# Kernel tuning notes

Hardware: AMD Instinct MI355X
Metric: run time of the kernel (lower is better)

Reference implementation:

```python
import jax, jax.numpy as jnp
import numpy as np

B, N, C, H = 8, 1024, 768, 12
D = C // H
HID = 4 * C
MAX_TEXT_LEN = 512
LN_EPS = 1e-5


def _ln(x, g, b):
    mu = jnp.mean(x, axis=-1, keepdims=True)
    var = jnp.mean(jnp.square(x - mu), axis=-1, keepdims=True)
    return (x - mu) * jax.lax.rsqrt(var + LN_EPS) * g + b


def _mlp(x, w1, b1, w2, b2):
    h = jax.nn.gelu(x @ w1.T + b1, approximate=False)
    return h @ w2.T + b2


def setup_inputs() -> dict:
    key = jax.random.key(0)
    ks = jax.random.split(key, 16)
    s = 0.02
    return {
        "x": jax.random.normal(ks[0], (B, N, C), jnp.float32),
        "mask": jax.random.randint(ks[1], (B, N), 0, 2).astype(bool),
        "rel_bias": jax.random.normal(ks[2], (H, N, N), jnp.float32) * s,
        "w_qkv": jax.random.normal(ks[3], (3 * C, C), jnp.float32) * s,
        "q_bias": jnp.zeros((C,), jnp.float32),
        "v_bias": jnp.zeros((C,), jnp.float32),
        "w_proj": jax.random.normal(ks[4], (C, C), jnp.float32) * s,
        "b_proj": jnp.zeros((C,), jnp.float32),
        "ln1_g": jnp.ones((C,), jnp.float32),
        "ln1_b": jnp.zeros((C,), jnp.float32),
        "ln2t_g": jnp.ones((C,), jnp.float32),
        "ln2t_b": jnp.zeros((C,), jnp.float32),
        "ln2i_g": jnp.ones((C,), jnp.float32),
        "ln2i_b": jnp.zeros((C,), jnp.float32),
        "w1t": jax.random.normal(ks[5], (HID, C), jnp.float32) * s,
        "b1t": jnp.zeros((HID,), jnp.float32),
        "w2t": jax.random.normal(ks[6], (C, HID), jnp.float32) * s,
        "b2t": jnp.zeros((C,), jnp.float32),
        "w1i": jax.random.normal(ks[7], (HID, C), jnp.float32) * s,
        "b1i": jnp.zeros((HID,), jnp.float32),
        "w2i": jax.random.normal(ks[8], (C, HID), jnp.float32) * s,
        "b2i": jnp.zeros((C,), jnp.float32),
        "gamma1": jnp.full((C,), 0.1, jnp.float32),
        "gamma2": jnp.full((C,), 0.1, jnp.float32),
    }


def reference(x, mask, rel_bias, w_qkv, q_bias, v_bias, w_proj, b_proj,
              ln1_g, ln1_b, ln2t_g, ln2t_b, ln2i_g, ln2i_b,
              w1t, b1t, w2t, b2t, w1i, b1i, w2i, b2i, gamma1, gamma2):
    # ---- attention branch ----
    h = _ln(x, ln1_g, ln1_b)
    qkv_bias = jnp.concatenate([q_bias, jnp.zeros_like(v_bias), v_bias])
    qkv = h @ w_qkv.T + qkv_bias                      # [B,N,3C]
    qkv = qkv.reshape(B, N, 3, H, D).transpose(2, 0, 3, 1, 4)  # [3,B,H,N,D]
    q, k, v = qkv[0], qkv[1], qkv[2]
    q = q * (D ** -0.5)
    attn = jnp.einsum('bhnd,bhmd->bhnm',
                      q.astype(jnp.float32), k.astype(jnp.float32))
    attn = attn + rel_bias[None]                      # [B,H,N,N]
    attn = jnp.where(mask[:, None, None, :], attn, -jnp.inf)
    attn = jax.nn.softmax(attn, axis=-1).astype(x.dtype)
    out = jnp.einsum('bhnm,bhmd->bhnd', attn, v)
    out = out.transpose(0, 2, 1, 3).reshape(B, N, C)
    out = out @ w_proj.T + b_proj
    x = x + gamma1 * out
    # ---- dual-branch layer-scaled MLP (mlp_vl is None path) ----
    xt = x[:, :MAX_TEXT_LEN]
    xi = x[:, MAX_TEXT_LEN:]
    xt = xt + gamma2 * _mlp(_ln(xt, ln2t_g, ln2t_b), w1t, b1t, w2t, b2t)
    xi = xi + gamma2 * _mlp(_ln(xi, ln2i_g, ln2i_b), w1i, b1i, w2i, b2i)
    return jnp.concatenate([xt, xi], axis=1)
```

## Files before the change

kernel.cpp:

```cpp
#include <hip/hip_runtime.h>
#include <hip/hip_bf16.h>
#include <math.h>

#define B_    8
#define N_TOK 1024
#define C_    768
#define H_    12
#define D_    64
#define HID_  3072

typedef __attribute__((ext_vector_type(4)))  float f32x4;
typedef __attribute__((ext_vector_type(16))) float f32x16;
typedef __attribute__((ext_vector_type(8)))  short s16x8;
typedef __attribute__((ext_vector_type(4)))  unsigned short u16x4;

static __device__ __forceinline__ unsigned short f2bf(float x){
  union { __hip_bfloat16 h; unsigned short u; } cv;
  cv.h = __float2bfloat16(x);
  return cv.u;
}
static __device__ __forceinline__ float bf2f(unsigned short u){
  return __uint_as_float(((unsigned)u) << 16);
}

#define GLOAD_LDS16(gp, lp) \
  __builtin_amdgcn_global_load_lds((const __attribute__((address_space(1))) unsigned int*)(gp), \
                                   (__attribute__((address_space(3))) unsigned int*)(lp), 16, 0, 0)

__global__ __launch_bounds__(256) void k_cvt(const float* __restrict__ src,
                                             unsigned short* __restrict__ dst, int n4){
  int i = blockIdx.x * 256 + threadIdx.x;
  if (i >= n4) return;
  const float4* s4 = (const float4*)src;
  float4 v = s4[i];
  u16x4 r;
  r.x = f2bf(v.x); r.y = f2bf(v.y); r.z = f2bf(v.z); r.w = f2bf(v.w);
  *(u16x4*)(dst + (size_t)i*4) = r;
}

__global__ __launch_bounds__(256) void k_ln1(const float* __restrict__ x,
                                             const float* __restrict__ g,
                                             const float* __restrict__ bta,
                                             unsigned short* __restrict__ out){
  int row  = blockIdx.x*4 + (threadIdx.x >> 6);
  int lane = threadIdx.x & 63;
  const float* xr = x + (size_t)row*C_;
  float v[12]; float s = 0.f;
  #pragma unroll
  for (int i=0;i<12;i++){ v[i] = xr[lane + i*64]; s += v[i]; }
  #pragma unroll
  for (int m=1;m<64;m<<=1) s += __shfl_xor(s, m);
  float mu = s * (1.f/768.f);
  float vs = 0.f;
  #pragma unroll
  for (int i=0;i<12;i++){ float d = v[i]-mu; vs += d*d; }
  #pragma unroll
  for (int m=1;m<64;m<<=1) vs += __shfl_xor(vs, m);
  float rs = rsqrtf(vs*(1.f/768.f) + 1e-5f);
  unsigned short* orow = out + (size_t)row*C_;
  #pragma unroll
  for (int i=0;i<12;i++){ int c = lane + i*64; orow[c] = f2bf((v[i]-mu)*rs*g[c] + bta[c]); }
}

__global__ __launch_bounds__(256) void k_ln2(const float* __restrict__ xmid,
                                             const float* __restrict__ gt, const float* __restrict__ bt,
                                             const float* __restrict__ gi, const float* __restrict__ bi,
                                             unsigned short* __restrict__ outc){
  int row  = blockIdx.x*4 + (threadIdx.x >> 6);
  int lane = threadIdx.x & 63;
  int bb = row >> 10, n = row & 1023;
  const float* G = (n < 512) ? gt : gi;
  const float* Bb = (n < 512) ? bt : bi;
  int crow = (n < 512) ? (bb*512 + n) : (4096 + bb*512 + (n - 512));
  const float* xr = xmid + (size_t)row*C_;
  float v[12]; float s = 0.f;
  #pragma unroll
  for (int i=0;i<12;i++){ v[i] = xr[lane + i*64]; s += v[i]; }
  #pragma unroll
  for (int m=1;m<64;m<<=1) s += __shfl_xor(s, m);
  float mu = s * (1.f/768.f);
  float vs = 0.f;
  #pragma unroll
  for (int i=0;i<12;i++){ float d = v[i]-mu; vs += d*d; }
  #pragma unroll
  for (int m=1;m<64;m<<=1) vs += __shfl_xor(vs, m);
  float rs = rsqrtf(vs*(1.f/768.f) + 1e-5f);
  unsigned short* orow = outc + (size_t)crow*C_;
  #pragma unroll
  for (int i=0;i<12;i++){ int c = lane + i*64; orow[c] = f2bf((v[i]-mu)*rs*G[c] + Bb[c]); }
}

template<int MODE>
__global__ __launch_bounds__(256) void k_gemm(
    const unsigned short* __restrict__ A,
    const unsigned short* __restrict__ Bw,
    int K,
    const float* __restrict__ bias,
    const float* __restrict__ bias2,
    const float* __restrict__ resid,
    const float* __restrict__ gamma,
    unsigned short* __restrict__ out_bf,
    float* __restrict__ out_f,
    int n_off)
{
  __shared__ __align__(16) char smem[32768];
  char* As = smem;
  char* Bs = smem + 16384;
  const int tid = threadIdx.x;
  const int lane = tid & 63, w = tid >> 6;
  const int wr = w >> 1, wc = w & 1;
  const int g16 = lane >> 4, c16 = lane & 15;
  const int row0 = blockIdx.x * 128, col0 = blockIdx.y * 128;

  f32x4 acc[4][4] = {};

  const char* Abase = (const char*)A;
  const char* Bbase = (const char*)Bw;
  const size_t rowbytes = (size_t)K * 2;

  for (int kt = 0; kt < K; kt += 64){
    __syncthreads();
    #pragma unroll
    for (int it = 0; it < 4; it++){
      int L = it*4096 + tid*16;
      int r = L >> 7, cb = L & 127;
      int scb = cb ^ ((r & 7) << 4);
      GLOAD_LDS16(Abase + (size_t)(row0 + r)*rowbytes + (size_t)kt*2 + scb, As + L);
      GLOAD_LDS16(Bbase + (size_t)(col0 + r)*rowbytes + (size_t)kt*2 + scb, Bs + L);
    }
    __syncthreads();

    s16x8 af[2][4], bfr[2][4];
    #pragma unroll
    for (int kk = 0; kk < 2; kk++){
      #pragma unroll
      for (int i = 0; i < 4; i++){
        int ra = wr*64 + i*16 + c16;
        af[kk][i]  = *(const s16x8*)(As + ra*128 + ((kk*64 + g16*16) ^ ((ra & 7) << 4)));
        int rb = wc*64 + i*16 + c16;
        bfr[kk][i] = *(const s16x8*)(Bs + rb*128 + ((kk*64 + g16*16) ^ ((rb & 7) << 4)));
      }
    }
    #pragma unroll
    for (int kk = 0; kk < 2; kk++)
      #pragma unroll
      for (int mi = 0; mi < 4; mi++)
        #pragma unroll
        for (int ni = 0; ni < 4; ni++)
          acc[mi][ni] = __builtin_amdgcn_mfma_f32_16x16x32_bf16(af[kk][mi], bfr[kk][ni], acc[mi][ni], 0, 0, 0);
  }

  #pragma unroll
  for (int mi = 0; mi < 4; mi++){
    int mbase = row0 + wr*64 + mi*16 + g16*4;
    #pragma unroll
    for (int ni = 0; ni < 4; ni++){
      int j = col0 + wc*64 + ni*16 + c16;
      f32x4 a = acc[mi][ni];
      if (MODE == 0){
        int which = j / 768;
        int cj = j - which*768;
        float bs = (which == 0) ? bias[cj] : (which == 2 ? bias2[cj] : 0.f);
        int head = cj >> 6, d = cj & 63;
        #pragma unroll
        for (int r = 0; r < 4; r++){
          int mm = mbase + r;
          int bb = mm >> 10, n = mm & 1023;
          float val = a[r] + bs;
          if (which == 0) val *= 0.125f;
          out_bf[((((size_t)which*B_ + bb)*H_ + head)*N_TOK + n)*D_ + d] = f2bf(val);
        }
      } else if (MODE == 1){
        float gm = gamma[j], bs = bias[j];
        #pragma unroll
        for (int r = 0; r < 4; r++){
          size_t idx = (size_t)(mbase + r)*C_ + j;
          out_f[idx] = resid[idx] + gm*(a[r] + bs);
        }
      } else if (MODE == 2){
        float bs = bias[j];
        #pragma unroll
        for (int r = 0; r < 4; r++){
          float t = a[r] + bs;
          out_bf[(size_t)(mbase + r)*HID_ + j] = f2bf(0.5f*t*(1.f + erff(t*0.70710678118654752f)));
        }
      } else {
        float gm = gamma[j], bs = bias[j];
        #pragma unroll
        for (int r = 0; r < 4; r++){
          int mm = mbase + r;
          int bb = mm >> 9, n = (mm & 511) + n_off;
          size_t idx = ((size_t)bb*N_TOK + n)*C_ + j;
          out_f[idx] = resid[idx] + gm*(a[r] + bs);
        }
      }
    }
  }
}

__global__ __launch_bounds__(256, 2) void k_attn(
    const unsigned short* __restrict__ qb,
    const unsigned short* __restrict__ kb,
    const unsigned short* __restrict__ vb,
    const unsigned short* __restrict__ bias_bf,
    const int* __restrict__ mask,
    unsigned short* __restrict__ outb)
{
  __shared__ __align__(16) char smem[45056];
  char* Vt0 = smem;
  char* Vt1 = smem + 8192;
  char* Ks  = smem + 16384;
  char* Bs  = smem + 24576;
  float* maskf = (float*)(smem + 40960);
  char* Oep = smem;

  int wg = blockIdx.x;
  int x = wg & 7, rest = wg >> 3;
  int qt = rest & 7, gl = rest >> 3;
  int g = gl*8 + x;
  int h = g % 12, bb = g / 12;

  const int tid = threadIdx.x, lane = tid & 63, w = tid >> 6;
  const int l31 = lane & 31, h5 = lane >> 5;
  const size_t bh = (size_t)bb*H_ + h;
  const char* qp = (const char*)(qb + bh*N_TOK*D_);
  const char* kp = (const char*)(kb + bh*N_TOK*D_);
  const unsigned short* vp = vb + bh*N_TOK*D_;
  const char* bp = (const char*)(bias_bf + (size_t)h*N_TOK*N_TOK);
  const int q0 = qt*128;
  const int qrow = q0 + w*32 + l31;
  const int qr = w*32 + l31;

  #pragma unroll
  for (int it = 0; it < 2; it++){
    int L = it*4096 + tid*16; int r = L >> 7, cb = L & 127;
    GLOAD_LDS16(kp + (size_t)r*128 + (cb ^ ((r & 7) << 4)), Ks + L);
  }
  #pragma unroll
  for (int it = 0; it < 4; it++){
    int L = it*4096 + tid*16; int r = L >> 7, cb = L & 127;
    GLOAD_LDS16(bp + (size_t)(q0 + r)*2048 + (cb ^ ((r & 7) << 4)), Bs + L);
  }
  unsigned short vv[16];
  #pragma unroll
  for (int j = 0; j < 16; j++) vv[j] = vp[(size_t)(w*16 + j)*D_ + lane];
  {
    int4 m4 = *(const int4*)(mask + bb*N_TOK + tid*4);
    float4 f4;
    f4.x = m4.x ? 0.f : -1e30f; f4.y = m4.y ? 0.f : -1e30f;
    f4.z = m4.z ? 0.f : -1e30f; f4.w = m4.w ? 0.f : -1e30f;
    *(float4*)(maskf + tid*4) = f4;
  }
  s16x8 qf[4];
  #pragma unroll
  for (int t = 0; t < 4; t++)
    qf[t] = *(const s16x8*)(qp + (size_t)qrow*128 + t*32 + h5*16);
  #pragma unroll
  for (int i = 0; i < 2; i++){
    s16x8 pk;
    #pragma unroll
    for (int e = 0; e < 8; e++) pk[e] = (short)vv[i*8 + e];
    *(s16x8*)(Vt0 + lane*128 + ((w*32 + i*16) ^ ((lane & 7) << 4))) = pk;
  }
  __syncthreads();

  f32x16 oacc[2] = {};
  float mrow = -1e30f, lrow = 0.f;

  for (int t = 0; t < 16; t++){
    const int kt = t*64;
    char* Vbuf = (t & 1) ? Vt1 : Vt0;
    char* Vnxt = (t & 1) ? Vt0 : Vt1;

    s16x8 kfr[2][4];
    #pragma unroll
    for (int ck = 0; ck < 2; ck++)
      #pragma unroll
      for (int tt = 0; tt < 4; tt++)
        kfr[ck][tt] = *(const s16x8*)(Ks + (ck*32 + l31)*128 + ((tt*32 + h5*16) ^ ((l31 & 7) << 4)));
    u16x4 bv[2][4];
    #pragma unroll
    for (int ck = 0; ck < 2; ck++)
      #pragma unroll
      for (int rq = 0; rq < 4; rq++){
        int off = ck*64 + rq*16 + h5*8;
        bv[ck][rq] = *(const u16x4*)(Bs + qr*128 + (off ^ ((qr & 7) << 4)));
      }
    __syncthreads();

    if (t < 15){
      #pragma unroll
      for (int it = 0; it < 2; it++){
        int L = it*4096 + tid*16; int r = L >> 7, cb = L & 127;
        GLOAD_LDS16(kp + (size_t)(kt + 64 + r)*128 + (cb ^ ((r & 7) << 4)), Ks + L);
      }
      #pragma unroll
      for (int it = 0; it < 4; it++){
        int L = it*4096 + tid*16; int r = L >> 7, cb = L & 127;
        GLOAD_LDS16(bp + (size_t)(q0 + r)*2048 + (size_t)(kt + 64)*2 + (cb ^ ((r & 7) << 4)), Bs + L);
      }
      #pragma unroll
      for (int j = 0; j < 16; j++)
        vv[j] = vp[(size_t)(kt + 64 + w*16 + j)*D_ + lane];
    }

    f32x16 sacc[2] = {};
    __builtin_amdgcn_s_setprio(1);
    #pragma unroll
    for (int tt = 0; tt < 4; tt++){
      sacc[0] = __builtin_amdgcn_mfma_f32_32x32x16_bf16(kfr[0][tt], qf[tt], sacc[0], 0, 0, 0);
      sacc[1] = __builtin_amdgcn_mfma_f32_32x32x16_bf16(kfr[1][tt], qf[tt], sacc[1], 0, 0, 0);
    }
    __builtin_amdgcn_s_setprio(0);

    float sv[2][16];
    #pragma unroll
    for (int ck = 0; ck < 2; ck++){
      #pragma unroll
      for (int r = 0; r < 16; r++){
        int kk = ck*32 + (r & 3) + 8*(r >> 2) + 4*h5;
        sv[ck][r] = sacc[ck][r] + bf2f(bv[ck][r >> 2][r & 3]) + maskf[kt + kk];
      }
    }

    float tmax = -1e30f;
    #pragma unroll
    for (int ck = 0; ck < 2; ck++)
      #pragma unroll
      for (int r = 0; r < 16; r++) tmax = fmaxf(tmax, sv[ck][r]);
    tmax = fmaxf(tmax, __shfl_xor(tmax, 32));
    float mnew = fmaxf(mrow, tmax);
    float sc = __expf(mrow - mnew);
    mrow = mnew;
    float ps = 0.f;
    #pragma unroll
    for (int ck = 0; ck < 2; ck++)
      #pragma unroll
      for (int r = 0; r < 16; r++){
        float p = __expf(sv[ck][r] - mnew);
        sv[ck][r] = p;
        ps += p;
      }
    ps += __shfl_xor(ps, 32);
    lrow = lrow*sc + ps;
    #pragma unroll
    for (int dt = 0; dt < 2; dt++)
      #pragma unroll
      for (int r = 0; r < 16; r++) oacc[dt][r] *= sc;

    #pragma unroll
    for (int ck = 0; ck < 2; ck++){
      #pragma unroll
      for (int kh = 0; kh < 2; kh++){
        unsigned wA, wB, wC, wD;
        asm("v_cvt_pk_bf16_f32 %0, %1, %2" : "=v"(wA) : "v"(sv[ck][kh*8+0]), "v"(sv[ck][kh*8+1]));
        asm("v_cvt_pk_bf16_f32 %0, %1, %2" : "=v"(wB) : "v"(sv[ck][kh*8+2]), "v"(sv[ck][kh*8+3]));
        asm("v_cvt_pk_bf16_f32 %0, %1, %2" : "=v"(wC) : "v"(sv[ck][kh*8+4]), "v"(sv[ck][kh*8+5]));
        asm("v_cvt_pk_bf16_f32 %0, %1, %2" : "=v"(wD) : "v"(sv[ck][kh*8+6]), "v"(sv[ck][kh*8+7]));
        unsigned tA = (unsigned)__shfl_xor((int)wA, 32);
        unsigned tB = (unsigned)__shfl_xor((int)wB, 32);
        unsigned tC = (unsigned)__shfl_xor((int)wC, 32);
        unsigned tD = (unsigned)__shfl_xor((int)wD, 32);
        union { unsigned u[4]; s16x8 v; } pu;
        pu.u[0] = h5 ? tC : wA;
        pu.u[1] = h5 ? tD : wB;
        pu.u[2] = h5 ? wC : tA;
        pu.u[3] = h5 ? wD : tB;
        __builtin_amdgcn_s_setprio(1);
        #pragma unroll
        for (int dt = 0; dt < 2; dt++){
          int d = dt*32 + l31;
          s16x8 vf = *(const s16x8*)(Vbuf + d*128 + ((ck*64 + kh*32 + h5*16) ^ ((d & 7) << 4)));
          oacc[dt] = __builtin_amdgcn_mfma_f32_32x32x16_bf16(vf, pu.v, oacc[dt], 0, 0, 0);
        }
        __builtin_amdgcn_s_setprio(0);
      }
    }

    if (t < 15){
      #pragma unroll
      for (int i = 0; i < 2; i++){
        s16x8 pk;
        #pragma unroll
        for (int e = 0; e < 8; e++) pk[e] = (short)vv[i*8 + e];
        *(s16x8*)(Vnxt + lane*128 + ((w*32 + i*16) ^ ((lane & 7) << 4))) = pk;
      }
    }
    __syncthreads();
  }

  float inv = 1.f / lrow;
  char* Ow = Oep + w*8192;
  #pragma unroll
  for (int dt = 0; dt < 2; dt++)
    #pragma unroll
    for (int r = 0; r < 16; r++){
      int d = dt*32 + (r & 3) + 8*(r >> 2) + 4*h5;
      *(float*)(Ow + l31*256 + ((d*4) ^ ((l31 & 7) << 4))) = oacc[dt][r] * inv;
    }
  int q2 = lane >> 1, dh = lane & 1;
  float of[32];
  #pragma unroll
  for (int i = 0; i < 8; i++){
    f32x4 v4 = *(const f32x4*)(Ow + q2*256 + ((dh*128 + i*16) ^ ((q2 & 7) << 4)));
    of[i*4+0] = v4[0]; of[i*4+1] = v4[1]; of[i*4+2] = v4[2]; of[i*4+3] = v4[3];
  }
  unsigned short* orow = outb + ((size_t)bb*N_TOK + q0 + w*32 + q2)*C_ + h*64 + dh*32;
  #pragma unroll
  for (int i = 0; i < 4; i++){
    s16x8 ob;
    #pragma unroll
    for (int e = 0; e < 8; e++) ob[e] = (short)f2bf(of[i*8+e]);
    *(s16x8*)(orow + i*8) = ob;
  }
}

extern "C" void kernel_launch(void* const* d_in, const int* in_sizes, int n_in,
                              void* d_out, int out_size, void* d_ws, size_t ws_size,
                              hipStream_t stream) {
  const float* x      = (const float*)d_in[0];
  const int*   mask   = (const int*)  d_in[1];
  const float* relb   = (const float*)d_in[2];
  const float* w_qkv  = (const float*)d_in[3];
  const float* q_bias = (const float*)d_in[4];
  const float* v_bias = (const float*)d_in[5];
  const float* w_proj = (const float*)d_in[6];
  const float* b_proj = (const float*)d_in[7];
  const float* ln1_g  = (const float*)d_in[8];
  const float* ln1_b  = (const float*)d_in[9];
  const float* ln2t_g = (const float*)d_in[10];
  const float* ln2t_b = (const float*)d_in[11];
  const float* ln2i_g = (const float*)d_in[12];
  const float* ln2i_b = (const float*)d_in[13];
  const float* w1t    = (const float*)d_in[14];
  const float* b1t    = (const float*)d_in[15];
  const float* w2t    = (const float*)d_in[16];
  const float* b2t    = (const float*)d_in[17];
  const float* w1i    = (const float*)d_in[18];
  const float* b1i    = (const float*)d_in[19];
  const float* w2i    = (const float*)d_in[20];
  const float* b2i    = (const float*)d_in[21];
  const float* gamma1 = (const float*)d_in[22];
  const float* gamma2 = (const float*)d_in[23];
  float* out = (float*)d_out;
  char* ws = (char*)d_ws;

  size_t off = 0;
  auto nxt = [&](size_t b){ size_t r = off; off += (b + 255) & ~(size_t)255; return r; };
  unsigned short* wq_bf  = (unsigned short*)(ws + nxt((size_t)3*C_*C_*2));
  unsigned short* wp_bf  = (unsigned short*)(ws + nxt((size_t)C_*C_*2));
  unsigned short* w1t_bf = (unsigned short*)(ws + nxt((size_t)HID_*C_*2));
  unsigned short* w2t_bf = (unsigned short*)(ws + nxt((size_t)HID_*C_*2));
  unsigned short* w1i_bf = (unsigned short*)(ws + nxt((size_t)HID_*C_*2));
  unsigned short* w2i_bf = (unsigned short*)(ws + nxt((size_t)HID_*C_*2));
  unsigned short* hln    = (unsigned short*)(ws + nxt((size_t)B_*N_TOK*C_*2));
  unsigned short* qkv    = (unsigned short*)(ws + nxt((size_t)3*B_*N_TOK*C_*2));
  unsigned short* attno  = (unsigned short*)(ws + nxt((size_t)B_*N_TOK*C_*2));
  float*          xmid   = (float*)(ws + nxt((size_t)B_*N_TOK*C_*4));
  unsigned short* ln2c   = hln;
  unsigned short* hidden = qkv;
  unsigned short* bias_bf = (unsigned short*)xmid;

  k_cvt<<<dim3((3*C_*C_/4 + 255)/256), 256, 0, stream>>>(w_qkv, wq_bf, 3*C_*C_/4);
  k_cvt<<<dim3((C_*C_/4 + 255)/256),   256, 0, stream>>>(w_proj, wp_bf, C_*C_/4);
  k_cvt<<<dim3((HID_*C_/4 + 255)/256), 256, 0, stream>>>(w1t, w1t_bf, HID_*C_/4);
  k_cvt<<<dim3((HID_*C_/4 + 255)/256), 256, 0, stream>>>(w2t, w2t_bf, HID_*C_/4);
  k_cvt<<<dim3((HID_*C_/4 + 255)/256), 256, 0, stream>>>(w1i, w1i_bf, HID_*C_/4);
  k_cvt<<<dim3((HID_*C_/4 + 255)/256), 256, 0, stream>>>(w2i, w2i_bf, HID_*C_/4);
  k_cvt<<<dim3((H_*N_TOK*N_TOK/4 + 255)/256), 256, 0, stream>>>(relb, bias_bf, H_*N_TOK*N_TOK/4);

  k_ln1<<<dim3(B_*N_TOK/4), 256, 0, stream>>>(x, ln1_g, ln1_b, hln);

  k_gemm<0><<<dim3(64, 18), 256, 0, stream>>>(hln, wq_bf, C_, q_bias, v_bias,
                                              nullptr, nullptr, qkv, nullptr, 0);

  const size_t qsz = (size_t)B_*H_*N_TOK*D_;
  k_attn<<<dim3(768), 256, 0, stream>>>(qkv, qkv + qsz, qkv + 2*qsz, bias_bf, mask, attno);

  k_gemm<1><<<dim3(64, 6), 256, 0, stream>>>(attno, wp_bf, C_, b_proj, nullptr,
                                             x, gamma1, nullptr, xmid, 0);

  k_ln2<<<dim3(B_*N_TOK/4), 256, 0, stream>>>(xmid, ln2t_g, ln2t_b, ln2i_g, ln2i_b, ln2c);

  k_gemm<2><<<dim3(32, 24), 256, 0, stream>>>(ln2c, w1t_bf, C_, b1t, nullptr,
                                              nullptr, nullptr, hidden, nullptr, 0);
  k_gemm<2><<<dim3(32, 24), 256, 0, stream>>>(ln2c + (size_t)4096*C_, w1i_bf, C_, b1i, nullptr,
                                              nullptr, nullptr, hidden + (size_t)4096*HID_, nullptr, 0);

  k_gemm<3><<<dim3(32, 6), 256, 0, stream>>>(hidden, w2t_bf, HID_, b2t, nullptr,
                                             xmid, gamma2, nullptr, out, 0);
  k_gemm<3><<<dim3(32, 6), 256, 0, stream>>>(hidden + (size_t)4096*HID_, w2i_bf, HID_, b2i, nullptr,
                                             xmid, gamma2, nullptr, out, 512);
}
```

Baseline: 372.9 us.

## Pipeline GEMM K-loop with 4-slot LDS ring and merge dual-branch MLP launches

Rewrites the GEMM main loop to use a 4-deep ring of 32-wide K slices in LDS. Three stages are prefetched ahead, with explicit vmcnt waits and one barrier per step in place of the two syncthreads, and MFMA issue is wrapped in setprio. It also remaps workgroup IDs in an XCD-aware way to improve L2 locality, and merges the text and image MLP GEMMs into single launches using blockIdx.z. The cost is 64KB of LDS with 2 blocks per CU requested, plus more dependence on hand-tuned waitcnt correctness.

```diff
diff --git a/kernel.cpp b/kernel.cpp
--- a/kernel.cpp
+++ b/kernel.cpp
@@ -91,63 +91,92 @@
 }
 
 template<int MODE>
-__global__ __launch_bounds__(256) void k_gemm(
+__global__ __launch_bounds__(256, 2) void k_gemm2(
     const unsigned short* __restrict__ A,
-    const unsigned short* __restrict__ Bw,
+    const unsigned short* __restrict__ Bw0,
+    const unsigned short* __restrict__ Bw1,
     int K,
-    const float* __restrict__ bias,
-    const float* __restrict__ bias2,
+    const float* __restrict__ bias0,
+    const float* __restrict__ bias1,
+    const float* __restrict__ qb2,
     const float* __restrict__ resid,
     const float* __restrict__ gamma,
     unsigned short* __restrict__ out_bf,
-    float* __restrict__ out_f,
-    int n_off)
+    float* __restrict__ out_f)
 {
-  __shared__ __align__(16) char smem[32768];
-  char* As = smem;
-  char* Bs = smem + 16384;
+  __shared__ __align__(16) char smem[65536];
   const int tid = threadIdx.x;
   const int lane = tid & 63, w = tid >> 6;
   const int wr = w >> 1, wc = w & 1;
   const int g16 = lane >> 4, c16 = lane & 15;
-  const int row0 = blockIdx.x * 128, col0 = blockIdx.y * 128;
+
+  const int gx = gridDim.x;
+  const int nwg = gx * gridDim.y;
+  const int flat = blockIdx.y * gx + blockIdx.x;
+  const int nid = (flat & 7) * (nwg >> 3) + (flat >> 3);
+  const int bx = nid % gx, by = nid / gx;
+  const int z = blockIdx.z;
+  const int row0 = bx*128, col0 = by*128;
+
+  const unsigned short* Ap = A;
+  const unsigned short* Bp = Bw0;
+  const float* bias = bias0;
+  if (MODE == 2 || MODE == 3){
+    if (z){ Ap = A + (size_t)4096*K; Bp = Bw1; bias = bias1; }
+  }
+  const char* Abase = (const char*)Ap;
+  const char* Bbase = (const char*)Bp;
+  const size_t rowbytes = (size_t)K*2;
+  const int KT2 = K >> 5;
+
+  auto stage = [&](int h){
+    char* slot = smem + (h & 3)*16384;
+    size_t kb = (size_t)h*64;
+    #pragma unroll
+    for (int it = 0; it < 2; it++){
+      int L = it*4096 + tid*16;
+      int r = L >> 6, cb = L & 63;
+      int scb = cb ^ ((r & 6) << 3);
+      GLOAD_LDS16(Abase + (size_t)(row0 + r)*rowbytes + kb + scb, slot + L);
+    }
+    #pragma unroll
+    for (int it = 0; it < 2; it++){
+      int L = it*4096 + tid*16;
+      int r = L >> 6, cb = L & 63;
+      int scb = cb ^ ((r & 6) << 3);
+      GLOAD_LDS16(Bbase + (size_t)(col0 + r)*rowbytes + kb + scb, slot + 8192 + L);
+    }
+  };
+
+  stage(0); stage(1); stage(2);
+  asm volatile("s_waitcnt vmcnt(8)" ::: "memory");
+  __builtin_amdgcn_s_barrier();
 
   f32x4 acc[4][4] = {};
-
-  const char* Abase = (const char*)A;
-  const char* Bbase = (const char*)Bw;
-  const size_t rowbytes = (size_t)K * 2;
-
-  for (int kt = 0; kt < K; kt += 64){
-    __syncthreads();
-    #pragma unroll
-    for (int it = 0; it < 4; it++){
-      int L = it*4096 + tid*16;
-      int r = L >> 7, cb = L & 127;
-      int scb = cb ^ ((r & 7) << 4);
-      GLOAD_LDS16(Abase + (size_t)(row0 + r)*rowbytes + (size_t)kt*2 + scb, As + L);
-      GLOAD_LDS16(Bbase + (size_t)(col0 + r)*rowbytes + (size_t)kt*2 + scb, Bs + L);
-    }
-    __syncthreads();
-
-    s16x8 af[2][4], bfr[2][4];
-    #pragma unroll
-    for (int kk = 0; kk < 2; kk++){
-      #pragma unroll
-      for (int i = 0; i < 4; i++){
-        int ra = wr*64 + i*16 + c16;
-        af[kk][i]  = *(const s16x8*)(As + ra*128 + ((kk*64 + g16*16) ^ ((ra & 7) << 4)));
-        int rb = wc*64 + i*16 + c16;
-        bfr[kk][i] = *(const s16x8*)(Bs + rb*128 + ((kk*64 + g16*16) ^ ((rb & 7) << 4)));
-      }
-    }
-    #pragma unroll
-    for (int kk = 0; kk < 2; kk++)
-      #pragma unroll
-      for (int mi = 0; mi < 4; mi++)
-        #pragma unroll
-        for (int ni = 0; ni < 4; ni++)
-          acc[mi][ni] = __builtin_amdgcn_mfma_f32_16x16x32_bf16(af[kk][mi], bfr[kk][ni], acc[mi][ni], 0, 0, 0);
+  for (int h = 0; h < KT2; h++){
+    if (h + 3 < KT2) stage(h + 3);
+    char* slot = smem + (h & 3)*16384;
+    s16x8 af[4], bf[4];
+    #pragma unroll
+    for (int i = 0; i < 4; i++){
+      int ra = wr*64 + i*16 + c16;
+      af[i] = *(const s16x8*)(slot + ra*64 + ((g16*16) ^ ((ra & 6) << 3)));
+      int rb = wc*64 + i*16 + c16;
+      bf[i] = *(const s16x8*)(slot + 8192 + rb*64 + ((g16*16) ^ ((rb & 6) << 3)));
+    }
+    __builtin_amdgcn_s_setprio(1);
+    #pragma unroll
+    for (int mi = 0; mi < 4; mi++)
+      #pragma unroll
+      for (int ni = 0; ni < 4; ni++)
+        acc[mi][ni] = __builtin_amdgcn_mfma_f32_16x16x32_bf16(af[mi], bf[ni], acc[mi][ni], 0, 0, 0);
+    __builtin_amdgcn_s_setprio(0);
+    if (h + 1 < KT2){
+      if (h + 3 < KT2)      asm volatile("s_waitcnt vmcnt(8)" ::: "memory");
+      else if (h + 2 < KT2) asm volatile("s_waitcnt vmcnt(4)" ::: "memory");
+      else                  asm volatile("s_waitcnt vmcnt(0)" ::: "memory");
+      __builtin_amdgcn_s_barrier();
+    }
   }
 
   #pragma unroll
@@ -158,9 +187,9 @@
       int j = col0 + wc*64 + ni*16 + c16;
       f32x4 a = acc[mi][ni];
       if (MODE == 0){
-        int which = j / 768;
+        int which = (j >= 1536) ? 2 : (j >= 768 ? 1 : 0);
         int cj = j - which*768;
-        float bs = (which == 0) ? bias[cj] : (which == 2 ? bias2[cj] : 0.f);
+        float bs = (which == 0) ? bias0[cj] : (which == 2 ? qb2[cj] : 0.f);
         int head = cj >> 6, d = cj & 63;
         #pragma unroll
         for (int r = 0; r < 4; r++){
@@ -179,17 +208,18 @@
         }
       } else if (MODE == 2){
         float bs = bias[j];
+        unsigned short* outp = out_bf + (size_t)z*4096*HID_;
         #pragma unroll
         for (int r = 0; r < 4; r++){
           float t = a[r] + bs;
-          out_bf[(size_t)(mbase + r)*HID_ + j] = f2bf(0.5f*t*(1.f + erff(t*0.70710678118654752f)));
+          outp[(size_t)(mbase + r)*HID_ + j] = f2bf(0.5f*t*(1.f + erff(t*0.70710678118654752f)));
         }
       } else {
         float gm = gamma[j], bs = bias[j];
         #pragma unroll
         for (int r = 0; r < 4; r++){
           int mm = mbase + r;
-          int bb = mm >> 9, n = (mm & 511) + n_off;
+          int bb = mm >> 9, n = (mm & 511) + (z ? 512 : 0);
           size_t idx = ((size_t)bb*N_TOK + n)*C_ + j;
           out_f[idx] = resid[idx] + gm*(a[r] + bs);
         }
@@ -471,24 +501,24 @@
 
   k_ln1<<<dim3(B_*N_TOK/4), 256, 0, stream>>>(x, ln1_g, ln1_b, hln);
 
-  k_gemm<0><<<dim3(64, 18), 256, 0, stream>>>(hln, wq_bf, C_, q_bias, v_bias,
-                                              nullptr, nullptr, qkv, nullptr, 0);
+  k_gemm2<0><<<dim3(64, 18, 1), 256, 0, stream>>>(hln, wq_bf, nullptr, C_,
+                                                  q_bias, nullptr, v_bias,
+                                                  nullptr, nullptr, qkv, nullptr);
 
   const size_t qsz = (size_t)B_*H_*N_TOK*D_;
   k_attn<<<dim3(768), 256, 0, stream>>>(qkv, qkv + qsz, qkv + 2*qsz, bias_bf, mask, attno);
 
-  k_gemm<1><<<dim3(64, 6), 256, 0, stream>>>(attno, wp_bf, C_, b_proj, nullptr,
-                                             x, gamma1, nullptr, xmid, 0);
+  k_gemm2<1><<<dim3(64, 6, 1), 256, 0, stream>>>(attno, wp_bf, nullptr, C_,
+                                                 b_proj, nullptr, nullptr,
+                                                 x, gamma1, nullptr, xmid);
 
   k_ln2<<<dim3(B_*N_TOK/4), 256, 0, stream>>>(xmid, ln2t_g, ln2t_b, ln2i_g, ln2i_b, ln2c);
 
-  k_gemm<2><<<dim3(32, 24), 256, 0, stream>>>(ln2c, w1t_bf, C_, b1t, nullptr,
-                                              nullptr, nullptr, hidden, nullptr, 0);
-  k_gemm<2><<<dim3(32, 24), 256, 0, stream>>>(ln2c + (size_t)4096*C_, w1i_bf, C_, b1i, nullptr,
-                                              nullptr, nullptr, hidden + (size_t)4096*HID_, nullptr, 0);
-
-  k_gemm<3><<<dim3(32, 6), 256, 0, stream>>>(hidden, w2t_bf, HID_, b2t, nullptr,
-                                             xmid, gamma2, nullptr, out, 0);
-  k_gemm<3><<<dim3(32, 6), 256, 0, stream>>>(hidden + (size_t)4096*HID_, w2i_bf, HID_, b2i, nullptr,
-                                             xmid, gamma2, nullptr, out, 512);
-}
+  k_gemm2<2><<<dim3(32, 24, 2), 256, 0, stream>>>(ln2c, w1t_bf, w1i_bf, C_,
+                                                  b1t, b1i, nullptr,
+                                                  nullptr, nullptr, hidden, nullptr);
+
+  k_gemm2<3><<<dim3(32, 6, 2), 256, 0, stream>>>(hidden, w2t_bf, w2i_bf, HID_,
+                                                 b2t, b2i, nullptr,
+                                                 xmid, gamma2, nullptr, out);
+}
```

New measurement: 348.7 us. 6.5% less time.
